# Kernel tuning notes

Measured on AMD Instinct MI355X. Metric: run time of the kernel, lower is better.

## Reference

```python
import jax, jax.numpy as jnp
import numpy as np

B, C, H, I = 32, 8, 512, 512


def act(x):
    # CustomActivation == hardtanh: (|x+1| - |x-1|) / 2
    return (jnp.abs(x + 1.0) - jnp.abs(x - 1.0)) * 0.5


def setup_inputs() -> dict:
    key = jax.random.key(0)
    ks = jax.random.split(key, 12)
    inp = jax.random.normal(ks[0], (B, C, H, I), dtype=jnp.float32)
    p_mask = jax.random.normal(ks[1], (H, I), dtype=jnp.float32)
    # Wp: tril(randn) with diagonal filled to 1 (matches __init__ + the no_grad
    # tril/clamp projection in forward, which is a no-op right after init).
    Wp = jnp.tril(jax.random.normal(ks[2], (H, H), dtype=jnp.float32))
    Wp = Wp - jnp.diag(jnp.diag(Wp)) + jnp.eye(H, dtype=jnp.float32)
    Wp_diag = jnp.ones((H,), dtype=jnp.float32)
    Wzp = jax.random.normal(ks[3], (H, H), dtype=jnp.float32)
    s = 1.0 / np.sqrt(I)
    def lin(k):
        kw, kb = jax.random.split(k)
        W = jax.random.uniform(kw, (I, I), jnp.float32, -s, s)
        b = jax.random.uniform(kb, (I,), jnp.float32, -s, s)
        return W, b
    p_lin_w, p_lin_b = lin(ks[4])
    z_lin_w, z_lin_b = lin(ks[5])
    fc1_w, fc1_b = lin(ks[6])
    fc2_w, fc2_b = lin(ks[7])
    return {
        'input': inp, 'p_mask': p_mask, 'Wp': Wp, 'Wp_diag': Wp_diag, 'Wzp': Wzp,
        'p_lin_w': p_lin_w, 'p_lin_b': p_lin_b,
        'z_lin_w': z_lin_w, 'z_lin_b': z_lin_b,
        'fc1_w': fc1_w, 'fc1_b': fc1_b, 'fc2_w': fc2_w, 'fc2_b': fc2_b,
    }


def reference(input, p_mask, Wp, Wp_diag, Wzp,
              p_lin_w, p_lin_b, z_lin_w, z_lin_b,
              fc1_w, fc1_b, fc2_w, fc2_b):
    x = input * (1.0 / 5000.0)                      # [B,C,H,I]
    p_set = x * act(p_mask)                         # split_input, broadcast over B,C
    Wp_eff = Wp + jnp.diag(Wp_diag)                 # [H,H]
    # per-channel Wp @ p_set[c], batched over B and C in one GEMM
    tp = jnp.einsum('hk,bcki->bchi', Wp_eff, p_set)
    tp = act(act(tp) @ p_lin_w.T + p_lin_b)         # p_output_layer
    tz = jnp.einsum('hk,bchi->bchi', Wzp, tp)       # wait-free channel-batched GEMM
    tz = act(act(tz) @ z_lin_w.T + z_lin_b)         # z_output_layer
    # sum over in_channel (out_channel==1 so broadcast-accumulate == sum)
    combined = tp.sum(axis=1) + tz.sum(axis=1) + x[:, 0]  # [B,H,I]
    out = jax.nn.relu(combined @ fc1_w.T + fc1_b)
    out = out @ fc2_w.T + fc2_b
    return out
```

## Files before the change

kernel.cpp:

```cpp
#include <hip/hip_runtime.h>

namespace {

constexpr int Bn = 32, Cn = 8, Hn = 512, In = 512;
constexpr size_t HI = (size_t)Hn * In;
constexpr float SC = 1.0f / 5000.0f;

using s16x8 = __attribute__((ext_vector_type(8))) short;
using f32x4 = __attribute__((ext_vector_type(4))) float;

__device__ __forceinline__ float actf(float x) {
    return fminf(1.0f, fmaxf(-1.0f, x));
}

__device__ __forceinline__ unsigned short f2bf(float f) {
    unsigned u = __builtin_bit_cast(unsigned, f);
    u += 0x7FFFu + ((u >> 16) & 1u);
    return (unsigned short)(u >> 16);
}
__device__ __forceinline__ float bf2f(unsigned short h) {
    return __builtin_bit_cast(float, (unsigned)h << 16);
}

__device__ __forceinline__ void async16(const void* g, void* l) {
    __builtin_amdgcn_global_load_lds(
        (const __attribute__((address_space(1))) unsigned*)g,
        (__attribute__((address_space(3))) unsigned*)l, 16, 0, 0);
}

template<int EPI, bool TRI>
__global__ __launch_bounds__(256, 3) void mfma_gemm(
    const unsigned short* __restrict__ A,
    const unsigned short* __restrict__ Bt,
    const float* __restrict__ bias,
    const float* __restrict__ zrow,
    unsigned short* __restrict__ out0,
    unsigned short* __restrict__ out1,
    float* __restrict__ outf,
    size_t sA, size_t sB, size_t sC)
{
    __shared__ __align__(16) unsigned short As[128 * 32];
    __shared__ __align__(16) unsigned short Bs[128 * 32];

    const int tid  = threadIdx.x;
    const int wid  = tid >> 6, lane = tid & 63;
    const int wr   = wid >> 1, wc = wid & 1;
    const size_t zb = blockIdx.z;

    const char* Ab = (const char*)(A + zb * sA) + (size_t)blockIdx.y * 131072;
    const char* Bb = (const char*)(Bt + zb * sB) + (size_t)blockIdx.x * 131072;

    f32x4 acc[4][4] = {};

    const int o0  = tid * 16;
    const int r0s = o0 >> 6;
    const int c0s = o0 & 63;

    const int kSteps = TRI ? ((int)blockIdx.y + 1) * 4 : 16;

    for (int ks = 0; ks < kSteps; ++ks) {
        const int k0b = ks * 64;
        async16(Ab + (size_t)r0s * 1024 + k0b + c0s,        (char*)As + wid * 1024);
        async16(Ab + (size_t)(64 + r0s) * 1024 + k0b + c0s, (char*)As + 4096 + wid * 1024);
        async16(Bb + (size_t)r0s * 1024 + k0b + c0s,        (char*)Bs + wid * 1024);
        async16(Bb + (size_t)(64 + r0s) * 1024 + k0b + c0s, (char*)Bs + 4096 + wid * 1024);
        __syncthreads();

        s16x8 a[4], b[4];
        const int kc = (lane >> 4) * 16;
        const int ar = wr * 64 + (lane & 15);
        const int br = wc * 64 + (lane & 15);
        #pragma unroll
        for (int m = 0; m < 4; ++m)
            a[m] = *(const s16x8*)((const char*)As + (size_t)(ar + m * 16) * 64 + kc);
        #pragma unroll
        for (int n = 0; n < 4; ++n)
            b[n] = *(const s16x8*)((const char*)Bs + (size_t)(br + n * 16) * 64 + kc);
        #pragma unroll
        for (int m = 0; m < 4; ++m)
            #pragma unroll
            for (int n = 0; n < 4; ++n)
                acc[m][n] = __builtin_amdgcn_mfma_f32_16x16x32_bf16(a[m], b[n], acc[m][n], 0, 0, 0);
        __syncthreads();
    }

    const int cb = blockIdx.x * 128 + wc * 64 + (lane & 15);
    const int rb = blockIdx.y * 128 + wr * 64 + ((lane >> 4) << 2);
    #pragma unroll
    for (int m = 0; m < 4; ++m) {
        #pragma unroll
        for (int n = 0; n < 4; ++n) {
            const int c = cb + n * 16;
            #pragma unroll
            for (int j = 0; j < 4; ++j) {
                const int r = rb + m * 16 + j;
                float v = acc[m][n][j];
                const size_t idx = zb * sC + (size_t)r * 512 + c;
                if (EPI == 0) {
                    out0[idx] = f2bf(actf(v));
                } else if (EPI == 1) {
                    float tp = actf(v + bias[c]);
                    out0[idx] = f2bf(tp);
                    out1[idx] = f2bf(actf(zrow[r & 511] * tp));
                } else if (EPI == 2) {
                    out0[idx] = f2bf(actf(v + bias[c]));
                } else if (EPI == 3) {
                    out0[idx] = f2bf(fmaxf(v + bias[c], 0.0f));
                } else {
                    outf[idx] = v + bias[c];
                }
            }
        }
    }
}

__global__ __launch_bounds__(256) void reduce_both(
    const unsigned short* __restrict__ tp,
    const unsigned short* __restrict__ tz,
    const float* __restrict__ x0,
    unsigned short* __restrict__ comb)
{
    size_t idx = (size_t)blockIdx.x * 256 + threadIdx.x;
    size_t b = idx >> 16;
    size_t p = (idx & 65535) * 4;
    float4 xv = *(const float4*)&x0[(b * Cn) * HI + p];
    float s0 = xv.x * SC, s1 = xv.y * SC, s2 = xv.z * SC, s3 = xv.w * SC;
    #pragma unroll
    for (int c = 0; c < Cn; ++c) {
        size_t q = (b * Cn + c) * HI + p;
        ushort4 a = *(const ushort4*)&tp[q];
        ushort4 d = *(const ushort4*)&tz[q];
        s0 += bf2f(a.x) + bf2f(d.x);
        s1 += bf2f(a.y) + bf2f(d.y);
        s2 += bf2f(a.z) + bf2f(d.z);
        s3 += bf2f(a.w) + bf2f(d.w);
    }
    ushort4 o;
    o.x = f2bf(s0); o.y = f2bf(s1); o.z = f2bf(s2); o.w = f2bf(s3);
    *(ushort4*)&comb[b * HI + p] = o;
}

__global__ __launch_bounds__(256) void transpose_mask(
    const float* __restrict__ x, const float* __restrict__ mask,
    unsigned short* __restrict__ xst)
{
    __shared__ float t[64][65];
    const int bc = blockIdx.z;
    const int i0 = blockIdx.x * 64, k0 = blockIdx.y * 64;
    const int r4 = threadIdx.x >> 6, cc = threadIdx.x & 63;
    const float* xp = x + (size_t)bc * HI;
    #pragma unroll
    for (int it = 0; it < 16; ++it) {
        int kl = it * 4 + r4;
        size_t g = (size_t)(k0 + kl) * In + i0 + cc;
        t[kl][cc] = xp[g] * (actf(mask[g]) * SC);
    }
    __syncthreads();
    unsigned short* op = xst + (size_t)bc * HI;
    #pragma unroll
    for (int it = 0; it < 16; ++it) {
        int il = it * 4 + r4;
        op[(size_t)(i0 + il) * Hn + k0 + cc] = f2bf(t[cc][il]);
    }
}

__global__ __launch_bounds__(256) void prep_wpe_bf(
    const float* __restrict__ Wp, const float* __restrict__ Wpd,
    unsigned short* __restrict__ o)
{
    int idx = blockIdx.x * 256 + threadIdx.x;
    int i = idx >> 9, j = idx & 511;
    o[idx] = f2bf(Wp[idx] + (i == j ? Wpd[i] : 0.0f));
}

__global__ __launch_bounds__(256) void conv_bf(
    const float* __restrict__ s, unsigned short* __restrict__ o)
{
    int idx = blockIdx.x * 256 + threadIdx.x;
    o[idx] = f2bf(s[idx]);
}

__global__ __launch_bounds__(64) void rowsum(
    const float* __restrict__ W, float* __restrict__ zr)
{
    int h = blockIdx.x, l = threadIdx.x;
    float s = 0.0f;
    for (int k = l; k < Hn; k += 64) s += W[h * Hn + k];
    #pragma unroll
    for (int off = 32; off; off >>= 1) s += __shfl_down(s, off, 64);
    if (!l) zr[h] = s;
}

}

extern "C" void kernel_launch(void* const* d_in, const int* in_sizes, int n_in,
                              void* d_out, int out_size, void* d_ws, size_t ws_size,
                              hipStream_t stream)
{
    const float* input  = (const float*)d_in[0];
    const float* p_mask = (const float*)d_in[1];
    const float* Wp     = (const float*)d_in[2];
    const float* Wpd    = (const float*)d_in[3];
    const float* Wzp    = (const float*)d_in[4];
    const float* plw    = (const float*)d_in[5];
    const float* plb    = (const float*)d_in[6];
    const float* zlw    = (const float*)d_in[7];
    const float* zlb    = (const float*)d_in[8];
    const float* f1w    = (const float*)d_in[9];
    const float* f1b    = (const float*)d_in[10];
    const float* f2w    = (const float*)d_in[11];
    const float* f2b    = (const float*)d_in[12];

    constexpr size_t WB = 512 * 512 * 2;
    char* w = (char*)d_ws;
    auto alloc = [&](size_t bytes) { char* p = w; w += (bytes + 255) & ~255ull; return p; };

    unsigned short* Wpeb  = (unsigned short*)alloc(WB);
    unsigned short* plwb  = (unsigned short*)alloc(WB);
    unsigned short* zlwb  = (unsigned short*)alloc(WB);
    unsigned short* f1wb  = (unsigned short*)alloc(WB);
    unsigned short* f2wb  = (unsigned short*)alloc(WB);
    float*          zrw   = (float*)alloc(512 * 4);
    unsigned short* combb = (unsigned short*)alloc((size_t)Bn * HI * 2);
    unsigned short* out1  = (unsigned short*)alloc((size_t)Bn * HI * 2);

    size_t fixedB = (size_t)(w - (char*)d_ws);
    int chunk = 32;
    while (chunk > 1 &&
           fixedB + 4ull * (size_t)chunk * Cn * HI * 2 + 4096 > ws_size)
        chunk >>= 1;
    const size_t CB = (size_t)chunk * Cn * HI * 2;
    unsigned short* xst   = (unsigned short*)alloc(CB);
    unsigned short* tpact = (unsigned short*)alloc(CB);
    unsigned short* tpb   = (unsigned short*)alloc(CB);
    unsigned short* tzin  = (unsigned short*)alloc(CB);
    unsigned short* tzb   = xst;

    prep_wpe_bf<<<512 * 512 / 256, 256, 0, stream>>>(Wp, Wpd, Wpeb);
    conv_bf<<<1024, 256, 0, stream>>>(plw, plwb);
    conv_bf<<<1024, 256, 0, stream>>>(zlw, zlwb);
    conv_bf<<<1024, 256, 0, stream>>>(f1w, f1wb);
    conv_bf<<<1024, 256, 0, stream>>>(f2w, f2wb);
    rowsum<<<512, 64, 0, stream>>>(Wzp, zrw);

    for (int b0 = 0; b0 < Bn; b0 += chunk) {
        const int nc = chunk * Cn;
        const float* inp_c = input + (size_t)b0 * Cn * HI;

        transpose_mask<<<dim3(8, 8, nc), 256, 0, stream>>>(inp_c, p_mask, xst);
        mfma_gemm<0, true><<<dim3(4, 4, nc), 256, 0, stream>>>(
            Wpeb, xst, nullptr, nullptr, tpact, nullptr, nullptr, 0, HI, HI);
        mfma_gemm<1, false><<<dim3(4, nc * 4, 1), 256, 0, stream>>>(
            tpact, plwb, plb, zrw, tpb, tzin, nullptr, 0, 0, 0);
        mfma_gemm<2, false><<<dim3(4, nc * 4, 1), 256, 0, stream>>>(
            tzin, zlwb, zlb, nullptr, tzb, nullptr, nullptr, 0, 0, 0);
        reduce_both<<<chunk * 256, 256, 0, stream>>>(
            tpb, tzb, inp_c, combb + (size_t)b0 * HI);
    }

    mfma_gemm<3, false><<<dim3(4, 128, 1), 256, 0, stream>>>(
        combb, f1wb, f1b, nullptr, out1, nullptr, nullptr, 0, 0, 0);
    mfma_gemm<4, false><<<dim3(4, 128, 1), 256, 0, stream>>>(
        out1, f2wb, f2b, nullptr, nullptr, nullptr, (float*)d_out, 0, 0, 0);
}
```

Baseline: 588.2 us.

## Fuse channel reduction into p/z linear GEMMs with in-register channel loop

Replaces the separate p-linear and z-linear GEMMs plus the reduce_both kernel with a GEMM kernel that loops over the 8 channels per block and accumulates the activated outputs in registers. The first pass writes the z-input and an fp32 partial sum (tp sum plus the scaled input); the second pass adds the tz sum and writes the bf16 combined tensor. This removes the bf16 tp/tz intermediate writes and rereads, but each block now runs the channels serially, which cuts grid parallelism by 8x (512 blocks per launch at full chunk) and adds an fp32 partial buffer.

```diff
diff --git a/kernel.cpp b/kernel.cpp
--- a/kernel.cpp
+++ b/kernel.cpp
@@ -33,11 +33,9 @@
     const unsigned short* __restrict__ A,
     const unsigned short* __restrict__ Bt,
     const float* __restrict__ bias,
-    const float* __restrict__ zrow,
     unsigned short* __restrict__ out0,
-    unsigned short* __restrict__ out1,
     float* __restrict__ outf,
-    size_t sA, size_t sB, size_t sC)
+    size_t sB, size_t sC)
 {
     __shared__ __align__(16) unsigned short As[128 * 32];
     __shared__ __align__(16) unsigned short Bs[128 * 32];
@@ -47,7 +45,7 @@
     const int wr   = wid >> 1, wc = wid & 1;
     const size_t zb = blockIdx.z;
 
-    const char* Ab = (const char*)(A + zb * sA) + (size_t)blockIdx.y * 131072;
+    const char* Ab = (const char*)A + (size_t)blockIdx.y * 131072;
     const char* Bb = (const char*)(Bt + zb * sB) + (size_t)blockIdx.x * 131072;
 
     f32x4 acc[4][4] = {};
@@ -96,48 +94,111 @@
                 const int r = rb + m * 16 + j;
                 float v = acc[m][n][j];
                 const size_t idx = zb * sC + (size_t)r * 512 + c;
-                if (EPI == 0) {
-                    out0[idx] = f2bf(actf(v));
-                } else if (EPI == 1) {
-                    float tp = actf(v + bias[c]);
-                    out0[idx] = f2bf(tp);
-                    out1[idx] = f2bf(actf(zrow[r & 511] * tp));
-                } else if (EPI == 2) {
-                    out0[idx] = f2bf(actf(v + bias[c]));
-                } else if (EPI == 3) {
-                    out0[idx] = f2bf(fmaxf(v + bias[c], 0.0f));
-                } else {
-                    outf[idx] = v + bias[c];
+                if (EPI == 0)      out0[idx] = f2bf(actf(v));
+                else if (EPI == 3) out0[idx] = f2bf(fmaxf(v + bias[c], 0.0f));
+                else               outf[idx] = v + bias[c];
+            }
+        }
+    }
+}
+
+template<bool G3>
+__global__ __launch_bounds__(256, 3) void gemm_cloop(
+    const unsigned short* __restrict__ Ab0,
+    const unsigned short* __restrict__ Bw,
+    const float* __restrict__ bias,
+    const float* __restrict__ zrow,
+    const float* __restrict__ input,
+    float* __restrict__ combp,
+    unsigned short* __restrict__ aux)
+{
+    __shared__ __align__(16) unsigned short As[128 * 32];
+    __shared__ __align__(16) unsigned short Bs[128 * 32];
+
+    const int tid  = threadIdx.x;
+    const int wid  = tid >> 6, lane = tid & 63;
+    const int wr   = wid >> 1, wc = wid & 1;
+    const int b  = blockIdx.z;
+    const int rt = blockIdx.y;
+
+    const char* Abase = (const char*)Ab0 + ((size_t)b * Cn * HI + (size_t)rt * 128 * 512) * 2;
+    const char* Bb    = (const char*)Bw + (size_t)blockIdx.x * 131072;
+
+    const int o0  = tid * 16;
+    const int r0s = o0 >> 6;
+    const int c0s = o0 & 63;
+
+    const int cb = blockIdx.x * 128 + wc * 64 + (lane & 15);
+    const int rb = rt * 128 + wr * 64 + ((lane >> 4) << 2);
+
+    f32x4 comb[4][4] = {};
+
+    #pragma unroll 1
+    for (int c = 0; c < Cn; ++c) {
+        const char* Ab = Abase + (size_t)c * HI * 2;
+        f32x4 acc[4][4] = {};
+
+        for (int ks = 0; ks < 16; ++ks) {
+            const int k0b = ks * 64;
+            async16(Ab + (size_t)r0s * 1024 + k0b + c0s,        (char*)As + wid * 1024);
+            async16(Ab + (size_t)(64 + r0s) * 1024 + k0b + c0s, (char*)As + 4096 + wid * 1024);
+            async16(Bb + (size_t)r0s * 1024 + k0b + c0s,        (char*)Bs + wid * 1024);
+            async16(Bb + (size_t)(64 + r0s) * 1024 + k0b + c0s, (char*)Bs + 4096 + wid * 1024);
+            __syncthreads();
+
+            s16x8 a[4], b2[4];
+            const int kc = (lane >> 4) * 16;
+            const int ar = wr * 64 + (lane & 15);
+            const int br = wc * 64 + (lane & 15);
+            #pragma unroll
+            for (int m = 0; m < 4; ++m)
+                a[m] = *(const s16x8*)((const char*)As + (size_t)(ar + m * 16) * 64 + kc);
+            #pragma unroll
+            for (int n = 0; n < 4; ++n)
+                b2[n] = *(const s16x8*)((const char*)Bs + (size_t)(br + n * 16) * 64 + kc);
+            #pragma unroll
+            for (int m = 0; m < 4; ++m)
+                #pragma unroll
+                for (int n = 0; n < 4; ++n)
+                    acc[m][n] = __builtin_amdgcn_mfma_f32_16x16x32_bf16(a[m], b2[n], acc[m][n], 0, 0, 0);
+            __syncthreads();
+        }
+
+        #pragma unroll
+        for (int m = 0; m < 4; ++m)
+            #pragma unroll
+            for (int n = 0; n < 4; ++n) {
+                const int col = cb + n * 16;
+                const float bs = bias[col];
+                #pragma unroll
+                for (int j = 0; j < 4; ++j) {
+                    float v = actf(acc[m][n][j] + bs);
+                    comb[m][n][j] += v;
+                    if (!G3) {
+                        const int r = rb + m * 16 + j;
+                        aux[((size_t)(b * Cn + c)) * HI + (size_t)r * 512 + col] =
+                            f2bf(actf(zrow[r] * v));
+                    }
                 }
             }
+    }
+
+    #pragma unroll
+    for (int m = 0; m < 4; ++m)
+        #pragma unroll
+        for (int n = 0; n < 4; ++n) {
+            const int col = cb + n * 16;
+            #pragma unroll
+            for (int j = 0; j < 4; ++j) {
+                const int r = rb + m * 16 + j;
+                const size_t ci = (size_t)b * HI + (size_t)r * 512 + col;
+                if (!G3)
+                    combp[ci] = comb[m][n][j] +
+                                input[(size_t)b * Cn * HI + (size_t)r * 512 + col] * SC;
+                else
+                    aux[ci] = f2bf(combp[ci] + comb[m][n][j]);
+            }
         }
-    }
-}
-
-__global__ __launch_bounds__(256) void reduce_both(
-    const unsigned short* __restrict__ tp,
-    const unsigned short* __restrict__ tz,
-    const float* __restrict__ x0,
-    unsigned short* __restrict__ comb)
-{
-    size_t idx = (size_t)blockIdx.x * 256 + threadIdx.x;
-    size_t b = idx >> 16;
-    size_t p = (idx & 65535) * 4;
-    float4 xv = *(const float4*)&x0[(b * Cn) * HI + p];
-    float s0 = xv.x * SC, s1 = xv.y * SC, s2 = xv.z * SC, s3 = xv.w * SC;
-    #pragma unroll
-    for (int c = 0; c < Cn; ++c) {
-        size_t q = (b * Cn + c) * HI + p;
-        ushort4 a = *(const ushort4*)&tp[q];
-        ushort4 d = *(const ushort4*)&tz[q];
-        s0 += bf2f(a.x) + bf2f(d.x);
-        s1 += bf2f(a.y) + bf2f(d.y);
-        s2 += bf2f(a.z) + bf2f(d.z);
-        s3 += bf2f(a.w) + bf2f(d.w);
-    }
-    ushort4 o;
-    o.x = f2bf(s0); o.y = f2bf(s1); o.z = f2bf(s2); o.w = f2bf(s3);
-    *(ushort4*)&comb[b * HI + p] = o;
 }
 
 __global__ __launch_bounds__(256) void transpose_mask(
@@ -227,14 +288,13 @@
     size_t fixedB = (size_t)(w - (char*)d_ws);
     int chunk = 32;
     while (chunk > 1 &&
-           fixedB + 4ull * (size_t)chunk * Cn * HI * 2 + 4096 > ws_size)
+           fixedB + (size_t)chunk * (3ull * Cn * HI * 2 + HI * 4) + 4096 > ws_size)
         chunk >>= 1;
     const size_t CB = (size_t)chunk * Cn * HI * 2;
     unsigned short* xst   = (unsigned short*)alloc(CB);
     unsigned short* tpact = (unsigned short*)alloc(CB);
-    unsigned short* tpb   = (unsigned short*)alloc(CB);
     unsigned short* tzin  = (unsigned short*)alloc(CB);
-    unsigned short* tzb   = xst;
+    float*          combp = (float*)alloc((size_t)chunk * HI * 4);
 
     prep_wpe_bf<<<512 * 512 / 256, 256, 0, stream>>>(Wp, Wpd, Wpeb);
     conv_bf<<<1024, 256, 0, stream>>>(plw, plwb);
@@ -249,17 +309,16 @@
 
         transpose_mask<<<dim3(8, 8, nc), 256, 0, stream>>>(inp_c, p_mask, xst);
         mfma_gemm<0, true><<<dim3(4, 4, nc), 256, 0, stream>>>(
-            Wpeb, xst, nullptr, nullptr, tpact, nullptr, nullptr, 0, HI, HI);
-        mfma_gemm<1, false><<<dim3(4, nc * 4, 1), 256, 0, stream>>>(
-            tpact, plwb, plb, zrw, tpb, tzin, nullptr, 0, 0, 0);
-        mfma_gemm<2, false><<<dim3(4, nc * 4, 1), 256, 0, stream>>>(
-            tzin, zlwb, zlb, nullptr, tzb, nullptr, nullptr, 0, 0, 0);
-        reduce_both<<<chunk * 256, 256, 0, stream>>>(
-            tpb, tzb, inp_c, combb + (size_t)b0 * HI);
+            Wpeb, xst, nullptr, tpact, nullptr, HI, HI);
+        gemm_cloop<false><<<dim3(4, 4, chunk), 256, 0, stream>>>(
+            tpact, plwb, plb, zrw, inp_c, combp, tzin);
+        gemm_cloop<true><<<dim3(4, 4, chunk), 256, 0, stream>>>(
+            tzin, zlwb, zlb, nullptr, nullptr, combp,
+            combb + (size_t)b0 * HI);
     }
 
     mfma_gemm<3, false><<<dim3(4, 128, 1), 256, 0, stream>>>(
-        combb, f1wb, f1b, nullptr, out1, nullptr, nullptr, 0, 0, 0);
+        combb, f1wb, f1b, out1, nullptr, 0, 0);
     mfma_gemm<4, false><<<dim3(4, 128, 1), 256, 0, stream>>>(
-        out1, f2wb, f2b, nullptr, nullptr, nullptr, (float*)d_out, 0, 0, 0);
-}
+        out1, f2wb, f2b, nullptr, (float*)d_out, 0, 0);
+}
```

Result: slower. 776.3 us (+32.0%).
